# Kernel tuning notes

Measured on AMD Instinct MI355X. Metric: run time of the kernel, lower is better.

The kernel has to match this reference:

```python
import jax, jax.numpy as jnp
import numpy as np

B, A, D, REL, H = 8, 192, 128, 5, 128

def setup_inputs() -> dict:
    key = jax.random.key(0)
    ks = jax.random.split(key, 10)
    coord = jax.random.normal(ks[0], (B, A, D), jnp.float32)
    goal = jax.random.normal(ks[1], (B, A, D), jnp.float32)
    frontier = jax.random.normal(ks[2], (B, A, D), jnp.float32)
    rel_feat = jax.random.normal(ks[3], (B, A, A, REL), jnp.float32)
    rule_adj = jax.random.randint(ks[4], (B, A, A), 0, 2) > 0
    base_score = jax.random.normal(ks[5], (B, A, A), jnp.float32)
    graph_context = jax.random.normal(ks[6], (B, D), jnp.float32)
    fan_in = 6 * D + REL + D
    W1 = jax.random.normal(ks[7], (fan_in, H), jnp.float32) / np.sqrt(fan_in)
    b1 = jnp.zeros((H,), jnp.float32)
    W2 = jax.random.normal(ks[8], (H, 1), jnp.float32) / np.sqrt(H)
    b2 = jnp.zeros((1,), jnp.float32)
    return {"coord": coord, "goal": goal, "frontier": frontier, "rel_feat": rel_feat,
            "rule_adj": rule_adj, "base_score": base_score, "graph_context": graph_context,
            "W1": W1, "b1": b1, "W2": W2, "b2": b2}

def reference(coord, goal, frontier, rel_feat, rule_adj, base_score, graph_context, W1, b1, W2, b2):
    b, a, d = coord.shape
    def pair(x):
        xi = jnp.broadcast_to(x[:, :, None, :], (b, a, a, d))
        xj = jnp.broadcast_to(x[:, None, :, :], (b, a, a, d))
        return xi, xj
    ci, cj = pair(coord)
    gi, gj = pair(goal)
    fi, fj = pair(frontier)
    gc = jnp.broadcast_to(graph_context[:, None, None, :], (b, a, a, d))
    edge_in = jnp.concatenate([ci, cj, gi, gj, fi, fj, rel_feat, gc], axis=-1)  # [B,A,A,7D+rel]
    h = jax.nn.relu(edge_in @ W1 + b1)
    learned = (h @ W2 + b2)[..., 0]  # [B,A,A]
    score = base_score + learned
    score = jnp.where(rule_adj, score, jnp.float32(-1e9))
    weights = jax.nn.softmax(score, axis=-1)
    weights = weights * rule_adj.astype(weights.dtype)
    weights = weights / (weights.sum(axis=-1, keepdims=True) + 1e-8)
    return weights, score, learned
```

## Files before the change

### kernel.cpp

```cpp
#include <hip/hip_runtime.h>
#include <math.h>

#define NB 8
#define NA 192
#define ND 128
#define NREL 5
#define NH 128
#define ROWS 6
#define NROWBLK ((NB * NA) / ROWS)
#define NPBLK (NROWBLK * 2)

__global__ __launch_bounds__(256, 4) void precompute_P(
    const float* __restrict__ coord, const float* __restrict__ goal,
    const float* __restrict__ frontier, const float* __restrict__ gctx,
    const float* __restrict__ W1, const float* __restrict__ b1,
    float* __restrict__ PiP, float* __restrict__ PjTP, float* __restrict__ Gc)
{
    const int blk = blockIdx.x;
    const int tid = threadIdx.x;

    if (blk >= 2 * NROWBLK) {
        __shared__ float red[256];
        const int b = blk - 2 * NROWBLK;
        const int h = tid & 127, part = tid >> 7;
        const float* g = gctx + b * ND + part * 64;
        const float* w = W1 + (size_t)(6 * ND + NREL + part * 64) * NH + h;
        float acc = 0.f;
#pragma unroll 8
        for (int d = 0; d < 64; ++d) acc += g[d] * w[d * NH];
        red[tid] = acc;
        __syncthreads();
        if (part == 0) Gc[b * NH + h] = red[h] + red[h + 128] + b1[h];
        return;
    }

    const int rb = blk >> 1;
    const int kh = blk & 1;
    const int r0 = rb * ROWS;

    __shared__ __align__(16) float X[ROWS][192];

    for (int idx = tid; idx < ROWS * 192; idx += 256) {
        int r = idx / 192;
        int kk = idx - r * 192;
        int k = kh * 192 + kk;
        int s = k >> 7, d = k & 127;
        const float* src = (s == 0) ? coord : (s == 1) ? goal : frontier;
        X[r][kk] = src[(r0 + r) * ND + d];
    }
    __syncthreads();

    const int colLocal = tid & 127;
    const int role = tid >> 7;
    const int roleOff = role * 128;

    float acc[ROWS];
#pragma unroll
    for (int r = 0; r < ROWS; r++) acc[r] = 0.f;

    auto seg = [&](int kkStart, int sChunk, int dStart, int len) {
        const float* wb = W1 + (size_t)(sChunk * 256 + roleOff + dStart) * NH + colLocal;
#pragma unroll 4
        for (int t = 0; t < len; t += 4) {
            float w0 = wb[0 * NH];
            float w1 = wb[1 * NH];
            float w2 = wb[2 * NH];
            float w3 = wb[3 * NH];
            wb += 4 * NH;
#pragma unroll
            for (int r = 0; r < ROWS; r++) {
                float4 x = *(const float4*)&X[r][kkStart + t];
                acc[r] += x.x * w0 + x.y * w1 + x.z * w2 + x.w * w3;
            }
        }
    };
    if (kh == 0) { seg(0, 0, 0, 128); seg(128, 1, 0, 64); }
    else         { seg(0, 1, 64, 64); seg(64, 2, 0, 128); }

#pragma unroll
    for (int r = 0; r < ROWS; r++) {
        int row = r0 + r;
        if (role == 0) {
            PiP[((size_t)kh * NB * NA + row) * NH + colLocal] = acc[r];
        } else {
            int b = row / NA, a = row - b * NA;
            PjTP[(((size_t)kh * NB + b) * NH + colLocal) * NA + a] = acc[r];
        }
    }
}

__global__ __launch_bounds__(192) void edge_kernel(
    const float* __restrict__ PiP, const float* __restrict__ PjTP,
    const float* __restrict__ Gc, const float* __restrict__ W1,
    const float* __restrict__ W2, const float* __restrict__ b2v,
    const float* __restrict__ rel_feat, const int* __restrict__ rule_adj,
    const float* __restrict__ base_score,
    float* __restrict__ out_w, float* __restrict__ out_s, float* __restrict__ out_l)
{
    const int bi = blockIdx.x;
    const int b = bi / NA;
    const int tid = threadIdx.x;

    __shared__ float4 su1[NH];
    __shared__ float4 su2[NH];
    __shared__ float redA[3], redB[3], redC[3];

    if (tid < NH) {
        float pig = PiP[(size_t)bi * NH + tid]
                  + PiP[(size_t)(NB * NA + bi) * NH + tid]
                  + Gc[b * NH + tid];
        const float* wr = W1 + (size_t)(6 * ND) * NH + tid;
        su1[tid] = make_float4(pig, wr[0 * NH], wr[1 * NH], wr[2 * NH]);
        su2[tid] = make_float4(wr[3 * NH], wr[4 * NH], W2[tid], 0.f);
    }

    float rel[NREL];
    const float* rf = rel_feat + ((size_t)bi * NA + tid) * NREL;
#pragma unroll
    for (int r = 0; r < NREL; r++) rel[r] = rf[r];

    __syncthreads();

    const float* pj0 = PjTP + (size_t)b * NH * NA + tid;
    const float* pj1 = pj0 + (size_t)NB * NH * NA;
    float acc = 0.f;
#pragma unroll 8
    for (int h = 0; h < NH; ++h) {
        float p = pj0[h * NA] + pj1[h * NA];
        float4 a = su1[h];
        float4 c = su2[h];
        float pre = a.x + p;
        pre += rel[0] * a.y;
        pre += rel[1] * a.z;
        pre += rel[2] * a.w;
        pre += rel[3] * c.x;
        pre += rel[4] * c.y;
        acc += fmaxf(pre, 0.f) * c.z;
    }
    float learned = acc + b2v[0];
    out_l[(size_t)bi * NA + tid] = learned;

    const int adj = rule_adj[(size_t)bi * NA + tid];
    const float sc = adj ? (base_score[(size_t)bi * NA + tid] + learned) : -1e9f;
    out_s[(size_t)bi * NA + tid] = sc;

    const int wave = tid >> 6, lane = tid & 63;

    float m = sc;
#pragma unroll
    for (int off = 32; off > 0; off >>= 1) m = fmaxf(m, __shfl_xor(m, off, 64));
    if (lane == 0) redA[wave] = m;
    __syncthreads();
    m = fmaxf(fmaxf(redA[0], redA[1]), redA[2]);

    float e = __expf(sc - m);
    float S = e;
#pragma unroll
    for (int off = 32; off > 0; off >>= 1) S += __shfl_xor(S, off, 64);
    if (lane == 0) redB[wave] = S;
    __syncthreads();
    S = redB[0] + redB[1] + redB[2];

    float wj = adj ? e * (1.f / S) : 0.f;
    float sw = wj;
#pragma unroll
    for (int off = 32; off > 0; off >>= 1) sw += __shfl_xor(sw, off, 64);
    if (lane == 0) redC[wave] = sw;
    __syncthreads();
    sw = redC[0] + redC[1] + redC[2];

    out_w[(size_t)bi * NA + tid] = wj * (1.f / (sw + 1e-8f));
}

extern "C" void kernel_launch(void* const* d_in, const int* in_sizes, int n_in,
                              void* d_out, int out_size, void* d_ws, size_t ws_size,
                              hipStream_t stream) {
    const float* coord    = (const float*)d_in[0];
    const float* goal     = (const float*)d_in[1];
    const float* frontier = (const float*)d_in[2];
    const float* rel_feat = (const float*)d_in[3];
    const int*   rule_adj = (const int*)d_in[4];
    const float* base_sc  = (const float*)d_in[5];
    const float* gctx     = (const float*)d_in[6];
    const float* W1       = (const float*)d_in[7];
    const float* b1       = (const float*)d_in[8];
    const float* W2       = (const float*)d_in[9];
    const float* b2       = (const float*)d_in[10];

    float* PiP  = (float*)d_ws;
    float* PjTP = PiP + 2 * NB * NA * NH;
    float* Gc   = PjTP + 2 * NB * NH * NA;

    float* out_w = (float*)d_out;
    float* out_s = out_w + NB * NA * NA;
    float* out_l = out_s + NB * NA * NA;

    precompute_P<<<2 * NROWBLK + NB, 256, 0, stream>>>(coord, goal, frontier, gctx,
                                                       W1, b1, PiP, PjTP, Gc);
    edge_kernel<<<NB * NA, 192, 0, stream>>>(PiP, PjTP, Gc, W1, W2, b2, rel_feat,
                                             rule_adj, base_sc, out_w, out_s, out_l);
}
```

Measured before the change: 116.8 us.

## Split projection K four ways, pre-reduce Pj, tile two rows per edge block

The precompute kernel now splits the 384-wide K dimension into four quarters instead of two, doubling the number of blocks. A new combine kernel sums the four Pj partials into one transposed buffer. The edge kernel processes two query rows per block with 384 threads: the hidden dimension is split across two halves, and each Pj load is reused for both rows before partial sums are combined in shared memory. This cuts Pj global reads and the number of blocks, at the cost of an extra kernel launch, more workspace traffic and serialized per-row softmax with extra barriers.

Result: no change. 118.8 us (+1.7%).

```diff
diff --git a/kernel.cpp b/kernel.cpp
--- a/kernel.cpp
+++ b/kernel.cpp
@@ -7,8 +7,9 @@
 #define NREL 5
 #define NH 128
 #define ROWS 6
+#define KS 4
 #define NROWBLK ((NB * NA) / ROWS)
-#define NPBLK (NROWBLK * 2)
+#define TI 2
 
 __global__ __launch_bounds__(256, 4) void precompute_P(
     const float* __restrict__ coord, const float* __restrict__ goal,
@@ -19,9 +20,9 @@
     const int blk = blockIdx.x;
     const int tid = threadIdx.x;
 
-    if (blk >= 2 * NROWBLK) {
+    if (blk >= KS * NROWBLK) {
         __shared__ float red[256];
-        const int b = blk - 2 * NROWBLK;
+        const int b = blk - KS * NROWBLK;
         const int h = tid & 127, part = tid >> 7;
         const float* g = gctx + b * ND + part * 64;
         const float* w = W1 + (size_t)(6 * ND + NREL + part * 64) * NH + h;
@@ -34,16 +35,16 @@
         return;
     }
 
-    const int rb = blk >> 1;
-    const int kh = blk & 1;
+    const int rb = blk >> 2;
+    const int kq = blk & 3;
     const int r0 = rb * ROWS;
 
-    __shared__ __align__(16) float X[ROWS][192];
-
-    for (int idx = tid; idx < ROWS * 192; idx += 256) {
-        int r = idx / 192;
-        int kk = idx - r * 192;
-        int k = kh * 192 + kk;
+    __shared__ __align__(16) float X[ROWS][96];
+
+    for (int idx = tid; idx < ROWS * 96; idx += 256) {
+        int r = idx / 96;
+        int kk = idx - r * 96;
+        int k = kq * 96 + kk;
         int s = k >> 7, d = k & 127;
         const float* src = (s == 0) ? coord : (s == 1) ? goal : frontier;
         X[r][kk] = src[(r0 + r) * ND + d];
@@ -74,102 +75,139 @@
             }
         }
     };
-    if (kh == 0) { seg(0, 0, 0, 128); seg(128, 1, 0, 64); }
-    else         { seg(0, 1, 64, 64); seg(64, 2, 0, 128); }
+    if (kq == 0)      { seg(0, 0, 0, 96); }
+    else if (kq == 1) { seg(0, 0, 96, 32); seg(32, 1, 0, 64); }
+    else if (kq == 2) { seg(0, 1, 64, 64); seg(64, 2, 0, 32); }
+    else              { seg(0, 2, 32, 96); }
 
 #pragma unroll
     for (int r = 0; r < ROWS; r++) {
         int row = r0 + r;
         if (role == 0) {
-            PiP[((size_t)kh * NB * NA + row) * NH + colLocal] = acc[r];
+            PiP[((size_t)kq * NB * NA + row) * NH + colLocal] = acc[r];
         } else {
             int b = row / NA, a = row - b * NA;
-            PjTP[(((size_t)kh * NB + b) * NH + colLocal) * NA + a] = acc[r];
-        }
-    }
-}
-
-__global__ __launch_bounds__(192) void edge_kernel(
-    const float* __restrict__ PiP, const float* __restrict__ PjTP,
+            PjTP[(((size_t)kq * NB + b) * NH + colLocal) * NA + a] = acc[r];
+        }
+    }
+}
+
+__global__ __launch_bounds__(256) void combine_PjT(
+    const float* __restrict__ PjTP, float* __restrict__ PjT)
+{
+    const size_t e = (size_t)blockIdx.x * 256 + threadIdx.x;
+    const size_t n = (size_t)NB * NH * NA;
+    float v = PjTP[e] + PjTP[n + e] + PjTP[2 * n + e] + PjTP[3 * n + e];
+    PjT[e] = v;
+}
+
+__global__ __launch_bounds__(384, 4) void edge_kernel(
+    const float* __restrict__ PiP, const float* __restrict__ PjT,
     const float* __restrict__ Gc, const float* __restrict__ W1,
     const float* __restrict__ W2, const float* __restrict__ b2v,
     const float* __restrict__ rel_feat, const int* __restrict__ rule_adj,
     const float* __restrict__ base_score,
     float* __restrict__ out_w, float* __restrict__ out_s, float* __restrict__ out_l)
 {
-    const int bi = blockIdx.x;
-    const int b = bi / NA;
+    const int b  = blockIdx.x / (NA / TI);
+    const int i0 = (blockIdx.x % (NA / TI)) * TI;
     const int tid = threadIdx.x;
-
-    __shared__ float4 su1[NH];
-    __shared__ float4 su2[NH];
+    const int j = tid % NA;
+    const int half = tid / NA;
+
+    __shared__ __align__(16) float4 su1[NH];
+    __shared__ __align__(16) float4 su2[NH];
+    __shared__ float s_part[2][TI][NA];
     __shared__ float redA[3], redB[3], redC[3];
 
     if (tid < NH) {
-        float pig = PiP[(size_t)bi * NH + tid]
-                  + PiP[(size_t)(NB * NA + bi) * NH + tid]
-                  + Gc[b * NH + tid];
-        const float* wr = W1 + (size_t)(6 * ND) * NH + tid;
-        su1[tid] = make_float4(pig, wr[0 * NH], wr[1 * NH], wr[2 * NH]);
-        su2[tid] = make_float4(wr[3 * NH], wr[4 * NH], W2[tid], 0.f);
-    }
-
-    float rel[NREL];
-    const float* rf = rel_feat + ((size_t)bi * NA + tid) * NREL;
-#pragma unroll
-    for (int r = 0; r < NREL; r++) rel[r] = rf[r];
-
+        const int h = tid;
+        const int row0 = b * NA + i0;
+        float pig0 = Gc[b * NH + h], pig1 = pig0;
+#pragma unroll
+        for (int kq = 0; kq < KS; ++kq) {
+            pig0 += PiP[((size_t)kq * NB * NA + row0) * NH + h];
+            pig1 += PiP[((size_t)kq * NB * NA + row0 + 1) * NH + h];
+        }
+        const float* wr = W1 + (size_t)(6 * ND) * NH + h;
+        su1[h] = make_float4(wr[0 * NH], wr[1 * NH], wr[2 * NH], wr[3 * NH]);
+        su2[h] = make_float4(wr[4 * NH], W2[h], pig0, pig1);
+    }
+
+    float r0v[NREL], r1v[NREL];
+    {
+        const float* rf0 = rel_feat + (((size_t)(b * NA + i0) * NA) + j) * NREL;
+        const float* rf1 = rf0 + (size_t)NA * NREL;
+#pragma unroll
+        for (int r = 0; r < NREL; r++) { r0v[r] = rf0[r]; r1v[r] = rf1[r]; }
+    }
     __syncthreads();
 
-    const float* pj0 = PjTP + (size_t)b * NH * NA + tid;
-    const float* pj1 = pj0 + (size_t)NB * NH * NA;
-    float acc = 0.f;
-#pragma unroll 8
-    for (int h = 0; h < NH; ++h) {
-        float p = pj0[h * NA] + pj1[h * NA];
-        float4 a = su1[h];
-        float4 c = su2[h];
-        float pre = a.x + p;
-        pre += rel[0] * a.y;
-        pre += rel[1] * a.z;
-        pre += rel[2] * a.w;
-        pre += rel[3] * c.x;
-        pre += rel[4] * c.y;
-        acc += fmaxf(pre, 0.f) * c.z;
-    }
-    float learned = acc + b2v[0];
-    out_l[(size_t)bi * NA + tid] = learned;
-
-    const int adj = rule_adj[(size_t)bi * NA + tid];
-    const float sc = adj ? (base_score[(size_t)bi * NA + tid] + learned) : -1e9f;
-    out_s[(size_t)bi * NA + tid] = sc;
+    const float* pjb = PjT + ((size_t)b * NH + half * 64) * NA + j;
+    float acc0 = 0.f, acc1 = 0.f;
+#pragma unroll 4
+    for (int hh = 0; hh < 64; ++hh) {
+        float p = pjb[hh * NA];
+        float4 a = su1[half * 64 + hh];
+        float4 c = su2[half * 64 + hh];
+        float pre0 = c.z + p;
+        pre0 += r0v[0] * a.x; pre0 += r0v[1] * a.y; pre0 += r0v[2] * a.z;
+        pre0 += r0v[3] * a.w; pre0 += r0v[4] * c.x;
+        float pre1 = c.w + p;
+        pre1 += r1v[0] * a.x; pre1 += r1v[1] * a.y; pre1 += r1v[2] * a.z;
+        pre1 += r1v[3] * a.w; pre1 += r1v[4] * c.x;
+        acc0 += fmaxf(pre0, 0.f) * c.y;
+        acc1 += fmaxf(pre1, 0.f) * c.y;
+    }
+    s_part[half][0][j] = acc0;
+    s_part[half][1][j] = acc1;
+    __syncthreads();
 
     const int wave = tid >> 6, lane = tid & 63;
-
-    float m = sc;
-#pragma unroll
-    for (int off = 32; off > 0; off >>= 1) m = fmaxf(m, __shfl_xor(m, off, 64));
-    if (lane == 0) redA[wave] = m;
-    __syncthreads();
-    m = fmaxf(fmaxf(redA[0], redA[1]), redA[2]);
-
-    float e = __expf(sc - m);
-    float S = e;
-#pragma unroll
-    for (int off = 32; off > 0; off >>= 1) S += __shfl_xor(S, off, 64);
-    if (lane == 0) redB[wave] = S;
-    __syncthreads();
-    S = redB[0] + redB[1] + redB[2];
-
-    float wj = adj ? e * (1.f / S) : 0.f;
-    float sw = wj;
-#pragma unroll
-    for (int off = 32; off > 0; off >>= 1) sw += __shfl_xor(sw, off, 64);
-    if (lane == 0) redC[wave] = sw;
-    __syncthreads();
-    sw = redC[0] + redC[1] + redC[2];
-
-    out_w[(size_t)bi * NA + tid] = wj * (1.f / (sw + 1e-8f));
+    const float b2c = b2v[0];
+    float scv[TI];
+    int adjv[TI];
+    if (tid < NA) {
+#pragma unroll
+        for (int ti = 0; ti < TI; ++ti) {
+            const size_t row = (size_t)(b * NA + i0 + ti) * NA + tid;
+            float lrn = s_part[0][ti][tid] + s_part[1][ti][tid] + b2c;
+            out_l[row] = lrn;
+            adjv[ti] = rule_adj[row];
+            scv[ti] = adjv[ti] ? (base_score[row] + lrn) : -1e9f;
+            out_s[row] = scv[ti];
+        }
+    }
+
+#pragma unroll
+    for (int ti = 0; ti < TI; ++ti) {
+        float m = (tid < NA) ? scv[ti] : -3.4e38f;
+#pragma unroll
+        for (int off = 32; off > 0; off >>= 1) m = fmaxf(m, __shfl_xor(m, off, 64));
+        if (lane == 0 && wave < 3) redA[wave] = m;
+        __syncthreads();
+        m = fmaxf(fmaxf(redA[0], redA[1]), redA[2]);
+
+        float e = (tid < NA) ? __expf(scv[ti] - m) : 0.f;
+        float S = e;
+#pragma unroll
+        for (int off = 32; off > 0; off >>= 1) S += __shfl_xor(S, off, 64);
+        if (lane == 0 && wave < 3) redB[wave] = S;
+        __syncthreads();
+        S = redB[0] + redB[1] + redB[2];
+
+        float wj = (tid < NA && adjv[ti]) ? e * (1.f / S) : 0.f;
+        float sw = wj;
+#pragma unroll
+        for (int off = 32; off > 0; off >>= 1) sw += __shfl_xor(sw, off, 64);
+        if (lane == 0 && wave < 3) redC[wave] = sw;
+        __syncthreads();
+        sw = redC[0] + redC[1] + redC[2];
+
+        if (tid < NA)
+            out_w[(size_t)(b * NA + i0 + ti) * NA + tid] = wj * (1.f / (sw + 1e-8f));
+        __syncthreads();
+    }
 }
 
 extern "C" void kernel_launch(void* const* d_in, const int* in_sizes, int n_in,
@@ -188,15 +226,17 @@
     const float* b2       = (const float*)d_in[10];
 
     float* PiP  = (float*)d_ws;
-    float* PjTP = PiP + 2 * NB * NA * NH;
-    float* Gc   = PjTP + 2 * NB * NH * NA;
+    float* PjTP = PiP + KS * NB * NA * NH;
+    float* PjT  = PjTP + KS * NB * NH * NA;
+    float* Gc   = PjT + NB * NH * NA;
 
     float* out_w = (float*)d_out;
     float* out_s = out_w + NB * NA * NA;
     float* out_l = out_s + NB * NA * NA;
 
-    precompute_P<<<2 * NROWBLK + NB, 256, 0, stream>>>(coord, goal, frontier, gctx,
-                                                       W1, b1, PiP, PjTP, Gc);
-    edge_kernel<<<NB * NA, 192, 0, stream>>>(PiP, PjTP, Gc, W1, W2, b2, rel_feat,
-                                             rule_adj, base_sc, out_w, out_s, out_l);
-}
+    precompute_P<<<KS * NROWBLK + NB, 256, 0, stream>>>(coord, goal, frontier, gctx,
+                                                        W1, b1, PiP, PjTP, Gc);
+    combine_PjT<<<(NB * NH * NA) / 256, 256, 0, stream>>>(PjTP, PjT);
+    edge_kernel<<<NB * (NA / TI), 384, 0, stream>>>(PiP, PjT, Gc, W1, W2, b2, rel_feat,
+                                                    rule_adj, base_sc, out_w, out_s, out_l);
+}
```
